# Kernel tuning notes

Measured on AMD Instinct MI355X. Metric: run time of the kernel, lower is better.

The kernel has to match this reference:

```python
import jax, jax.numpy as jnp
import numpy as np

B, T, DIN, DOUT, RANK, UDIM = 4, 2048, 4096, 4096, 2, 16

def setup_inputs() -> dict:
    key = jax.random.key(0)
    ks = jax.random.split(key, 8)
    return {
        "x": jax.random.normal(ks[0], (B, T, DIN), jnp.float32),
        "W": jax.random.normal(ks[1], (DOUT, DIN), jnp.float32) * 0.02,
        "b": jax.random.normal(ks[2], (DOUT,), jnp.float32) * 0.02,
        "U": jax.random.normal(ks[3], (DOUT, RANK), jnp.float32) * 0.02,
        "S": jax.random.normal(ks[4], (RANK, RANK), jnp.float32),
        "Vh": jax.random.normal(ks[5], (RANK, DIN), jnp.float32) * 0.02,
        "P": jax.random.normal(ks[6], (UDIM, RANK, RANK), jnp.float32),
        "v": jax.random.normal(ks[7], (UDIM,), jnp.float32),
    }

def reference(x, W, b, U, S, Vh, P, v):
    # R = sum_u v[u] * P[u]  (intended meaning of einsum('u,urr->rr'))
    R = jnp.einsum('u,uab->ab', v, P)                 # [rank, rank]
    base = jnp.einsum('btd,od->bto', x, W) + b        # frozen linear
    # x @ delta_W.T with delta_W = U @ S @ R @ Vh, chained low-rank:
    M = U @ S @ R                                     # [out, rank]
    t = jnp.einsum('btd,rd->btr', x, Vh)              # [B, T, rank]
    delta = jnp.einsum('btr,or->bto', t, M)           # [B, T, out]
    return base + delta
```

## Files before the change

kernel.cpp:

```cpp
#include <hip/hip_runtime.h>
#include <hip/hip_bf16.h>
#include <stdint.h>

typedef __hip_bfloat16 bf16;
typedef __attribute__((ext_vector_type(8))) short bf16x8;
typedef __attribute__((ext_vector_type(4))) float f32x4;

static constexpr int Mtot = 8192;
static constexpr int Ktot = 4096;
static constexpr int Ntot = 4096;
static constexpr int BM = 256, BN = 256, BK = 64;
static constexpr int NKT = Ktot / BK;
static constexpr int CAST_BLOCKS = (Mtot * Ktot / 8) / 256;
static constexpr int PREP_BLOCKS = (Ntot * Ktot / 8) / 256;

__device__ __forceinline__ void gl_lds16(const void* g, void* l) {
  __builtin_amdgcn_global_load_lds(
      (const __attribute__((address_space(1))) void*)g,
      (__attribute__((address_space(3))) void*)l,
      16, 0, 0);
}

__device__ __forceinline__ uint32_t bf16pair(float a, float b) {
  __hip_bfloat16 ha = __float2bfloat16(a), hb = __float2bfloat16(b);
  uint16_t ia, ib;
  __builtin_memcpy(&ia, &ha, 2);
  __builtin_memcpy(&ib, &hb, 2);
  return (uint32_t)ia | ((uint32_t)ib << 16);
}

__global__ __launch_bounds__(256) void prep_kernel(const float* __restrict__ x,
                                                   bf16* __restrict__ xb,
                                                   const float* __restrict__ W,
                                                   const float* __restrict__ U,
                                                   const float* __restrict__ S,
                                                   const float* __restrict__ Vh,
                                                   const float* __restrict__ P,
                                                   const float* __restrict__ v,
                                                   bf16* __restrict__ Wp) {
  const int bid = blockIdx.x;
  if (bid < CAST_BLOCKS) {
    size_t gid = (size_t)bid * 256 + threadIdx.x;
    size_t d0 = gid * 8;
    const float4 a = ((const float4*)(x + d0))[0];
    const float4 b = ((const float4*)(x + d0))[1];
    uint4 pk;
    pk.x = bf16pair(a.x, a.y);
    pk.y = bf16pair(a.z, a.w);
    pk.z = bf16pair(b.x, b.y);
    pk.w = bf16pair(b.z, b.w);
    ((uint4*)(xb + d0))[0] = pk;
  } else {
    float R0 = 0.f, R1 = 0.f, R2 = 0.f, R3 = 0.f;
#pragma unroll
    for (int u = 0; u < 16; ++u) {
      float vu = v[u];
      R0 += vu * P[u * 4 + 0];
      R1 += vu * P[u * 4 + 1];
      R2 += vu * P[u * 4 + 2];
      R3 += vu * P[u * 4 + 3];
    }
    float SR00 = S[0] * R0 + S[1] * R2, SR01 = S[0] * R1 + S[1] * R3;
    float SR10 = S[2] * R0 + S[3] * R2, SR11 = S[2] * R1 + S[3] * R3;

    int gid = (bid - CAST_BLOCKS) * 256 + threadIdx.x;
    int o = gid >> 9;
    int d0 = (gid & 511) << 3;
    float u0 = U[o * 2 + 0], u1 = U[o * 2 + 1];
    float M0 = u0 * SR00 + u1 * SR10;
    float M1 = u0 * SR01 + u1 * SR11;

    const float* wrow = W + (size_t)o * Ktot + d0;
    const float4 w0 = ((const float4*)wrow)[0];
    const float4 w1 = ((const float4*)wrow)[1];
    const float4 a0 = ((const float4*)(Vh + d0))[0];
    const float4 a1 = ((const float4*)(Vh + d0))[1];
    const float4 b0 = ((const float4*)(Vh + Ktot + d0))[0];
    const float4 b1 = ((const float4*)(Vh + Ktot + d0))[1];
    float val[8];
    val[0] = w0.x + M0 * a0.x + M1 * b0.x;
    val[1] = w0.y + M0 * a0.y + M1 * b0.y;
    val[2] = w0.z + M0 * a0.z + M1 * b0.z;
    val[3] = w0.w + M0 * a0.w + M1 * b0.w;
    val[4] = w1.x + M0 * a1.x + M1 * b1.x;
    val[5] = w1.y + M0 * a1.y + M1 * b1.y;
    val[6] = w1.z + M0 * a1.z + M1 * b1.z;
    val[7] = w1.w + M0 * a1.w + M1 * b1.w;
    uint4 pk;
    pk.x = bf16pair(val[0], val[1]);
    pk.y = bf16pair(val[2], val[3]);
    pk.z = bf16pair(val[4], val[5]);
    pk.w = bf16pair(val[6], val[7]);
    ((uint4*)(Wp + (size_t)o * Ktot + d0))[0] = pk;
  }
}


#define SCHEDB __builtin_amdgcn_sched_barrier(0)
#define BAR do { SCHEDB; __builtin_amdgcn_s_barrier(); SCHEDB; } while (0)
#define LG0 do { asm volatile("s_waitcnt lgkmcnt(0)" ::: "memory"); SCHEDB; } while (0)
#define LG8 do { asm volatile("s_waitcnt lgkmcnt(8)" ::: "memory"); } while (0)
#define WVM(n) do { asm volatile("s_waitcnt vmcnt(" #n ")" ::: "memory"); } while (0)

__global__ __launch_bounds__(512, 2) void gemm_kernel(const bf16* __restrict__ A,
                                                      const bf16* __restrict__ Bt,
                                                      const float* __restrict__ bias,
                                                      float* __restrict__ out) {
  __shared__ __align__(16) bf16 As[2][BM * BK];
  __shared__ __align__(16) bf16 Bs[2][BN * BK];

  const int tid = (int)threadIdx.x;
  const int lane = tid & 63;
  const int w = tid >> 6;
  const int wr = w >> 2;
  const int wc = w & 3;

  const int bid = (int)blockIdx.x;
  const int xcd = bid & 7;
  const int ord = bid >> 3;
  const int rnd = ord >> 5;
  const int slt = ord & 31;
  const int mt = rnd * 16 + (xcd >> 1) * 4 + (slt >> 3);
  const int nt = (xcd & 1) * 8 + (slt & 7);
  const int m0 = mt * BM;
  const int n0 = nt * BN;

  const int l8 = lane >> 3;
  const int swcol = ((lane & 7) ^ l8) << 3;
  const bf16* gA = A + (size_t)(m0 + w * 16 + l8) * Ktot + swcol;
  const bf16* gB = Bt + (size_t)(n0 + w * 16 + l8) * Ktot + swcol;

  const int fm = lane & 15;
  const int q = lane >> 4;
  const int rx = (fm & 7) << 4;
  const int clo = (q * 16) ^ (rx & 48);
  const int aoff0 = (wr * 128 + fm) * 128 + clo + (rx & 64);
  const int aoff1 = (wr * 128 + fm) * 128 + clo + (64 ^ (rx & 64));
  const int boff0 = (wc * 64 + fm) * 128 + clo + (rx & 64);
  const int boff1 = (wc * 64 + fm) * 128 + clo + (64 ^ (rx & 64));

#define STA(BUF, half, kt) do { \
    const bf16* _g = gA + (size_t)((half) * 128) * Ktot + (kt) * 64; \
    char* _l = (char*)(&As[BUF][0]) + (half) * 16384 + w * 2048; \
    gl_lds16(_g, _l); \
    gl_lds16(_g + (size_t)8 * Ktot, _l + 1024); \
  } while (0)
#define STB(BUF, half, kt) do { \
    const bf16* _g = gB + (size_t)((half) * 128) * Ktot + (kt) * 64; \
    char* _l = (char*)(&Bs[BUF][0]) + (half) * 16384 + w * 2048; \
    gl_lds16(_g, _l); \
    gl_lds16(_g + (size_t)8 * Ktot, _l + 1024); \
  } while (0)
#define STAGE_H(BUF, h, kt) do { \
    if ((h) == 0) STA(BUF, 0, kt); else if ((h) == 1) STA(BUF, 1, kt); \
    else if ((h) == 2) STB(BUF, 0, kt); else STB(BUF, 1, kt); } while (0)

#define RD_A(dst, BUF, mh) do { \
    const char* _p = (const char*)(&As[BUF][0]) + (mh) * 8192; \
    _Pragma("unroll") for (int _i = 0; _i < 4; ++_i) { \
      dst[_i][0] = *(const bf16x8*)(_p + _i * 2048 + aoff0); \
      dst[_i][1] = *(const bf16x8*)(_p + _i * 2048 + aoff1); \
    } } while (0)
#define RD_B(dst, BUF, nh) do { \
    const char* _p = (const char*)(&Bs[BUF][0]) + (nh) * 4096; \
    _Pragma("unroll") for (int _j = 0; _j < 2; ++_j) { \
      dst[_j][0] = *(const bf16x8*)(_p + _j * 2048 + boff0); \
      dst[_j][1] = *(const bf16x8*)(_p + _j * 2048 + boff1); \
    } } while (0)

#define MFMA_Q(AV, BV, MH, NH) do { \
    __builtin_amdgcn_s_setprio(1); \
    _Pragma("unroll") for (int _i = 0; _i < 4; ++_i) \
    _Pragma("unroll") for (int _j = 0; _j < 2; ++_j) { \
      acc[(MH) * 4 + _i][(NH) * 2 + _j] = __builtin_amdgcn_mfma_f32_16x16x32_bf16( \
          AV[_i][0], BV[_j][0], acc[(MH) * 4 + _i][(NH) * 2 + _j], 0, 0, 0); \
      acc[(MH) * 4 + _i][(NH) * 2 + _j] = __builtin_amdgcn_mfma_f32_16x16x32_bf16( \
          AV[_i][1], BV[_j][1], acc[(MH) * 4 + _i][(NH) * 2 + _j], 0, 0, 0); \
    } \
    __builtin_amdgcn_s_setprio(0); \
  } while (0)

  f32x4 acc[8][4];
#pragma unroll
  for (int i = 0; i < 8; ++i)
#pragma unroll
    for (int j = 0; j < 4; ++j) acc[i][j] = {0.f, 0.f, 0.f, 0.f};

  bf16x8 a[4][2], b0[2][2], b1[2][2];

  STAGE_H(0, 0, 0); STAGE_H(0, 1, 0); STAGE_H(0, 2, 0); STAGE_H(0, 3, 0);
  STAGE_H(1, 2, 1); STAGE_H(1, 3, 1); STAGE_H(1, 0, 1);
  WVM(6);
  BAR;

  for (int it = 0; it < 31; ++it) {
    const int k1 = 2 * it + 1;
    const int k2 = 2 * it + 2;
    const int k3 = 2 * it + 3;
    RD_A(a, 0, 0); RD_B(b0, 0, 0); STAGE_H(1, 1, k1); LG8;
    BAR; LG0; MFMA_Q(a, b0, 0, 0); BAR;
    RD_B(b1, 0, 1);
    BAR; LG0; MFMA_Q(a, b1, 0, 1); BAR;
    RD_A(a, 0, 1); STAGE_H(0, 2, k2);
    BAR; LG0; MFMA_Q(a, b0, 1, 0); BAR;
    STAGE_H(0, 3, k2);
    BAR; MFMA_Q(a, b1, 1, 1); SCHEDB; WVM(4); BAR;
    RD_A(a, 1, 0); RD_B(b0, 1, 0); STAGE_H(0, 0, k2); LG8;
    BAR; LG0; MFMA_Q(a, b0, 0, 0); BAR;
    RD_B(b1, 1, 1); STAGE_H(0, 1, k2);
    BAR; LG0; MFMA_Q(a, b1, 0, 1); BAR;
    RD_A(a, 1, 1); STAGE_H(1, 2, k3);
    BAR; LG0; MFMA_Q(a, b0, 1, 0); BAR;
    STAGE_H(1, 3, k3); STAGE_H(1, 0, k3);
    BAR; MFMA_Q(a, b1, 1, 1); SCHEDB; WVM(6); BAR;
  }

  RD_A(a, 0, 0); RD_B(b0, 0, 0); STAGE_H(1, 1, 63); LG8;
  BAR; LG0; MFMA_Q(a, b0, 0, 0); BAR;
  RD_B(b1, 0, 1);
  BAR; LG0; MFMA_Q(a, b1, 0, 1); BAR;
  RD_A(a, 0, 1);
  BAR; LG0; MFMA_Q(a, b0, 1, 0); BAR;
  BAR; MFMA_Q(a, b1, 1, 1); SCHEDB; WVM(0); BAR;
  RD_A(a, 1, 0); RD_B(b0, 1, 0);
  BAR; LG0; MFMA_Q(a, b0, 0, 0); BAR;
  RD_B(b1, 1, 1);
  BAR; LG0; MFMA_Q(a, b1, 0, 1); BAR;
  RD_A(a, 1, 1);
  BAR; LG0; MFMA_Q(a, b0, 1, 0); BAR;
  MFMA_Q(a, b1, 1, 1);

#pragma unroll
  for (int jb = 0; jb < 4; ++jb) {
    const int gn = n0 + wc * 64 + jb * 16 + fm;
    const float bj = bias[gn];
#pragma unroll
    for (int ia = 0; ia < 8; ++ia) {
      float* o = out + (size_t)(m0 + wr * 128 + ia * 16 + q * 4) * Ntot + gn;
#pragma unroll
      for (int r = 0; r < 4; ++r) o[(size_t)r * Ntot] = acc[ia][jb][r] + bj;
    }
  }

#undef STA
#undef STB
#undef STAGE_H
#undef RD_A
#undef RD_B
#undef MFMA_Q
}

extern "C" void kernel_launch(void* const* d_in, const int* in_sizes, int n_in,
                              void* d_out, int out_size, void* d_ws, size_t ws_size,
                              hipStream_t stream) {
  const float* x  = (const float*)d_in[0];
  const float* W  = (const float*)d_in[1];
  const float* b  = (const float*)d_in[2];
  const float* U  = (const float*)d_in[3];
  const float* S  = (const float*)d_in[4];
  const float* Vh = (const float*)d_in[5];
  const float* P  = (const float*)d_in[6];
  const float* v  = (const float*)d_in[7];
  float* out = (float*)d_out;

  bf16* xb = (bf16*)d_ws;
  bf16* Wp = (bf16*)((char*)d_ws + (size_t)Mtot * Ktot * 2);

  prep_kernel<<<CAST_BLOCKS + PREP_BLOCKS, 256, 0, stream>>>(x, xb, W, U, S, Vh, P, v, Wp);

  dim3 grid(Mtot / BM * (Ntot / BN));
  gemm_kernel<<<grid, 512, 0, stream>>>(xb, Wp, b, out);
}
```

Before: 515.5 us.

## Make GEMM persistent over two M tiles and double-buffer A fragment reads

The GEMM now launches 256 blocks, and each block computes two M tiles in sequence instead of one block per tile (512 blocks). This is meant to cut the wave-quantization tail and the per-block launch cost on 256 CUs. Inside the K loop, a second A register set (a2) is added so the next A fragment is read from LDS while MFMAs on the current one run, using partial lgkmcnt waits. The cost is more VGPR pressure and a serialized epilogue between the two tiles, and the changed wait counts risk LDS/global races.

```diff
diff --git a/kernel.cpp b/kernel.cpp
--- a/kernel.cpp
+++ b/kernel.cpp
@@ -99,6 +99,7 @@
 #define SCHEDB __builtin_amdgcn_sched_barrier(0)
 #define BAR do { SCHEDB; __builtin_amdgcn_s_barrier(); SCHEDB; } while (0)
 #define LG0 do { asm volatile("s_waitcnt lgkmcnt(0)" ::: "memory"); SCHEDB; } while (0)
+#define LGK8 do { asm volatile("s_waitcnt lgkmcnt(8)" ::: "memory"); SCHEDB; } while (0)
 #define LG8 do { asm volatile("s_waitcnt lgkmcnt(8)" ::: "memory"); } while (0)
 #define WVM(n) do { asm volatile("s_waitcnt vmcnt(" #n ")" ::: "memory"); } while (0)
 
@@ -118,17 +119,12 @@
   const int bid = (int)blockIdx.x;
   const int xcd = bid & 7;
   const int ord = bid >> 3;
-  const int rnd = ord >> 5;
-  const int slt = ord & 31;
-  const int mt = rnd * 16 + (xcd >> 1) * 4 + (slt >> 3);
-  const int nt = (xcd & 1) * 8 + (slt & 7);
-  const int m0 = mt * BM;
+  const int mtb = (xcd >> 1) * 4 + (ord >> 3);
+  const int nt  = (xcd & 1) * 8 + (ord & 7);
   const int n0 = nt * BN;
 
   const int l8 = lane >> 3;
   const int swcol = ((lane & 7) ^ l8) << 3;
-  const bf16* gA = A + (size_t)(m0 + w * 16 + l8) * Ktot + swcol;
-  const bf16* gB = Bt + (size_t)(n0 + w * 16 + l8) * Ktot + swcol;
 
   const int fm = lane & 15;
   const int q = lane >> 4;
@@ -181,64 +177,68 @@
   } while (0)
 
   f32x4 acc[8][4];
-#pragma unroll
-  for (int i = 0; i < 8; ++i)
-#pragma unroll
-    for (int j = 0; j < 4; ++j) acc[i][j] = {0.f, 0.f, 0.f, 0.f};
-
-  bf16x8 a[4][2], b0[2][2], b1[2][2];
-
-  STAGE_H(0, 0, 0); STAGE_H(0, 1, 0); STAGE_H(0, 2, 0); STAGE_H(0, 3, 0);
-  STAGE_H(1, 2, 1); STAGE_H(1, 3, 1); STAGE_H(1, 0, 1);
-  WVM(6);
-  BAR;
-
-  for (int it = 0; it < 31; ++it) {
-    const int k1 = 2 * it + 1;
-    const int k2 = 2 * it + 2;
-    const int k3 = 2 * it + 3;
-    RD_A(a, 0, 0); RD_B(b0, 0, 0); STAGE_H(1, 1, k1); LG8;
+  bf16x8 a[4][2], a2[4][2], b0[2][2], b1[2][2];
+
+  for (int rep = 0; rep < 2; ++rep) {
+    const int m0 = (mtb + rep * 16) * BM;
+    const bf16* gA = A + (size_t)(m0 + w * 16 + l8) * Ktot + swcol;
+    const bf16* gB = Bt + (size_t)(n0 + w * 16 + l8) * Ktot + swcol;
+
+#pragma unroll
+    for (int i = 0; i < 8; ++i)
+#pragma unroll
+      for (int j = 0; j < 4; ++j) acc[i][j] = {0.f, 0.f, 0.f, 0.f};
+
+    STAGE_H(0, 0, 0); STAGE_H(0, 1, 0); STAGE_H(0, 2, 0); STAGE_H(0, 3, 0);
+    STAGE_H(1, 2, 1); STAGE_H(1, 3, 1); STAGE_H(1, 0, 1);
+    WVM(6);
+    BAR;
+
+    for (int it = 0; it < 31; ++it) {
+      const int k1 = 2 * it + 1;
+      const int k2 = 2 * it + 2;
+      const int k3 = 2 * it + 3;
+      RD_A(a, 0, 0); RD_B(b0, 0, 0); STAGE_H(1, 1, k1); LG8;
+      BAR; LG0; MFMA_Q(a, b0, 0, 0); BAR;
+      RD_B(b1, 0, 1); SCHEDB; RD_A(a2, 0, 1);
+      BAR; LGK8; MFMA_Q(a, b1, 0, 1); BAR;
+      STAGE_H(0, 2, k2);
+      BAR; LG0; MFMA_Q(a2, b0, 1, 0); BAR;
+      STAGE_H(0, 3, k2);
+      BAR; MFMA_Q(a2, b1, 1, 1); SCHEDB; WVM(6); BAR;
+      RD_A(a, 1, 0); RD_B(b0, 1, 0); STAGE_H(0, 0, k2); LG8;
+      BAR; LG0; MFMA_Q(a, b0, 0, 0); SCHEDB; WVM(6); BAR;
+      RD_B(b1, 1, 1); SCHEDB; RD_A(a2, 1, 1); SCHEDB; STAGE_H(0, 1, k2);
+      BAR; LGK8; MFMA_Q(a, b1, 0, 1); BAR;
+      STAGE_H(1, 2, k3);
+      BAR; LG0; MFMA_Q(a2, b0, 1, 0); BAR;
+      STAGE_H(1, 3, k3); STAGE_H(1, 0, k3);
+      BAR; MFMA_Q(a2, b1, 1, 1); SCHEDB; WVM(6); BAR;
+    }
+
+    RD_A(a, 0, 0); RD_B(b0, 0, 0); STAGE_H(1, 1, 63); LG8;
     BAR; LG0; MFMA_Q(a, b0, 0, 0); BAR;
-    RD_B(b1, 0, 1);
-    BAR; LG0; MFMA_Q(a, b1, 0, 1); BAR;
-    RD_A(a, 0, 1); STAGE_H(0, 2, k2);
-    BAR; LG0; MFMA_Q(a, b0, 1, 0); BAR;
-    STAGE_H(0, 3, k2);
-    BAR; MFMA_Q(a, b1, 1, 1); SCHEDB; WVM(4); BAR;
-    RD_A(a, 1, 0); RD_B(b0, 1, 0); STAGE_H(0, 0, k2); LG8;
-    BAR; LG0; MFMA_Q(a, b0, 0, 0); BAR;
-    RD_B(b1, 1, 1); STAGE_H(0, 1, k2);
-    BAR; LG0; MFMA_Q(a, b1, 0, 1); BAR;
-    RD_A(a, 1, 1); STAGE_H(1, 2, k3);
-    BAR; LG0; MFMA_Q(a, b0, 1, 0); BAR;
-    STAGE_H(1, 3, k3); STAGE_H(1, 0, k3);
-    BAR; MFMA_Q(a, b1, 1, 1); SCHEDB; WVM(6); BAR;
-  }
-
-  RD_A(a, 0, 0); RD_B(b0, 0, 0); STAGE_H(1, 1, 63); LG8;
-  BAR; LG0; MFMA_Q(a, b0, 0, 0); BAR;
-  RD_B(b1, 0, 1);
-  BAR; LG0; MFMA_Q(a, b1, 0, 1); BAR;
-  RD_A(a, 0, 1);
-  BAR; LG0; MFMA_Q(a, b0, 1, 0); BAR;
-  BAR; MFMA_Q(a, b1, 1, 1); SCHEDB; WVM(0); BAR;
-  RD_A(a, 1, 0); RD_B(b0, 1, 0);
-  BAR; LG0; MFMA_Q(a, b0, 0, 0); BAR;
-  RD_B(b1, 1, 1);
-  BAR; LG0; MFMA_Q(a, b1, 0, 1); BAR;
-  RD_A(a, 1, 1);
-  BAR; LG0; MFMA_Q(a, b0, 1, 0); BAR;
-  MFMA_Q(a, b1, 1, 1);
-
-#pragma unroll
-  for (int jb = 0; jb < 4; ++jb) {
-    const int gn = n0 + wc * 64 + jb * 16 + fm;
-    const float bj = bias[gn];
-#pragma unroll
-    for (int ia = 0; ia < 8; ++ia) {
-      float* o = out + (size_t)(m0 + wr * 128 + ia * 16 + q * 4) * Ntot + gn;
-#pragma unroll
-      for (int r = 0; r < 4; ++r) o[(size_t)r * Ntot] = acc[ia][jb][r] + bj;
+    RD_B(b1, 0, 1); SCHEDB; RD_A(a2, 0, 1);
+    BAR; LGK8; MFMA_Q(a, b1, 0, 1); BAR;
+    BAR; LG0; MFMA_Q(a2, b0, 1, 0); BAR;
+    BAR; MFMA_Q(a2, b1, 1, 1); SCHEDB; WVM(2); BAR;
+    RD_A(a, 1, 0); RD_B(b0, 1, 0); LG8;
+    BAR; LG0; MFMA_Q(a, b0, 0, 0); SCHEDB; WVM(0); BAR;
+    RD_B(b1, 1, 1); SCHEDB; RD_A(a2, 1, 1);
+    BAR; LGK8; MFMA_Q(a, b1, 0, 1); BAR;
+    BAR; LG0; MFMA_Q(a2, b0, 1, 0); BAR;
+    MFMA_Q(a2, b1, 1, 1);
+
+#pragma unroll
+    for (int jb = 0; jb < 4; ++jb) {
+      const int gn = n0 + wc * 64 + jb * 16 + fm;
+      const float bj = bias[gn];
+#pragma unroll
+      for (int ia = 0; ia < 8; ++ia) {
+        float* o = out + (size_t)(m0 + wr * 128 + ia * 16 + q * 4) * Ntot + gn;
+#pragma unroll
+        for (int r = 0; r < 4; ++r) o[(size_t)r * Ntot] = acc[ia][jb][r] + bj;
+      }
     }
   }
 
@@ -268,6 +268,5 @@
 
   prep_kernel<<<CAST_BLOCKS + PREP_BLOCKS, 256, 0, stream>>>(x, xb, W, U, S, Vh, P, v, Wp);
 
-  dim3 grid(Mtot / BM * (Ntot / BN));
-  gemm_kernel<<<grid, 512, 0, stream>>>(xb, Wp, b, out);
-}
+  gemm_kernel<<<256, 512, 0, stream>>>(xb, Wp, b, out);
+}
```

Result: slower. 642.6 us (+24.6%).
